# Optimization experiments

Measured on AMD Instinct MI355X. Metric: run time of the kernel, lower is better.

## Reference

```python
import jax, jax.numpy as jnp
import numpy as np

D_K = 64
EPS = 1e-6


def setup_inputs() -> dict:
    key = jax.random.key(0)
    ks = jax.random.split(key, 6)
    B, S, D2, DV = 4, 2048, 1024, 64
    q = jax.random.normal(ks[0], (B, S, D2), dtype=jnp.float32)
    k = jax.random.normal(ks[1], (B, S, D2), dtype=jnp.float32)
    v = jax.random.normal(ks[2], (B, S, D2), dtype=jnp.float32)
    mask = jax.random.randint(ks[3], (B, S, S), 0, 2) == 1
    V = jax.random.normal(ks[4], (1, DV), dtype=jnp.float32)
    fc_w = jax.random.normal(ks[5], (D2, DV), dtype=jnp.float32) * (1.0 / np.sqrt(DV))
    fc_b = jnp.zeros((D2,), dtype=jnp.float32)
    ln_g = jnp.ones((D2,), dtype=jnp.float32)
    ln_b = jnp.zeros((D2,), dtype=jnp.float32)
    return {"q": q, "k": k, "v": v, "mask": mask, "V": V,
            "fc_w": fc_w, "fc_b": fc_b, "ln_g": ln_g, "ln_b": ln_b}


def _layer_norm(x, g, b):
    mu = jnp.mean(x, axis=-1, keepdims=True)
    var = jnp.var(x, axis=-1, keepdims=True)
    return (x - mu) * jax.lax.rsqrt(var + EPS) * g + b


def reference(q, k, v, mask, V, fc_w, fc_b, ln_g, ln_b):
    residual = q
    qn = _layer_norm(q, ln_g, ln_b)
    # scaled dot-product scores (no softmax in this variant)
    attn = jnp.einsum('bsd,btd->bst', qn / jnp.sqrt(jnp.float32(D_K)), k)
    attn = jnp.where(mask, 0.0, attn)  # masked_fill with 0
    # v_ = V broadcast over (batch, seq, key); attn @ v_ == row-sum outer V
    output = jnp.sum(attn, axis=-1, keepdims=True) * V  # [B,S,d_v]
    output = output @ fc_w.T + fc_b                     # [B,S,2*d_model]
    output = output + residual
    return (output, attn)
```

## Files before the change

kernel.cpp:

```cpp
#include <hip/hip_runtime.h>
#include <hip/hip_bf16.h>
#include <cstdint>

#define S_LEN 2048
#define D2_   1024
#define DV_   64
#define NB_   4

typedef __bf16 bf16x8 __attribute__((ext_vector_type(8)));
typedef float  f32x16 __attribute__((ext_vector_type(16)));

__device__ __forceinline__ unsigned short f2bf(float f) {
  union { float f; unsigned int u; } v; v.f = f;
  unsigned int r = v.u + 0x7fffu + ((v.u >> 16) & 1u);
  return (unsigned short)(r >> 16);
}

__device__ __forceinline__ void async16(const unsigned short* g, unsigned short* l) {
  __builtin_amdgcn_global_load_lds(
      (__attribute__((address_space(1))) void*)g,
      (__attribute__((address_space(3))) void*)l,
      16, 0, 0);
}

__global__ void __launch_bounds__(256) prep_kernel(
    const float* __restrict__ q, const float* __restrict__ k,
    const float* __restrict__ gam, const float* __restrict__ bet,
    const float* __restrict__ V, const float* __restrict__ fw,
    unsigned short* __restrict__ qn, unsigned short* __restrict__ kb,
    float* __restrict__ w2, float* __restrict__ rowsum) {
  const int row = blockIdx.x;
  const int t = threadIdx.x;

  if (row < 32) rowsum[row * 256 + t] = 0.0f;

  const float4 x = ((const float4*)(q + (size_t)row * D2_))[t];
  float s  = x.x + x.y + x.z + x.w;
  float ss = x.x * x.x + x.y * x.y + x.z * x.z + x.w * x.w;
  #pragma unroll
  for (int o = 32; o > 0; o >>= 1) { s += __shfl_down(s, o); ss += __shfl_down(ss, o); }
  __shared__ float red[8];
  if ((t & 63) == 0) { red[t >> 6] = s; red[(t >> 6) + 4] = ss; }
  __syncthreads();
  const float tot  = red[0] + red[1] + red[2] + red[3];
  const float tots = red[4] + red[5] + red[6] + red[7];
  const float mu  = tot * (1.0f / D2_);
  const float var = tots * (1.0f / D2_) - mu * mu;
  const float rs  = rsqrtf(var + 1e-6f) * 0.125f;
  const float4 gv = ((const float4*)gam)[t];
  const float4 bv = ((const float4*)bet)[t];
  ushort4 o4;
  o4.x = f2bf((x.x - mu) * rs * gv.x + 0.125f * bv.x);
  o4.y = f2bf((x.y - mu) * rs * gv.y + 0.125f * bv.y);
  o4.z = f2bf((x.z - mu) * rs * gv.z + 0.125f * bv.z);
  o4.w = f2bf((x.w - mu) * rs * gv.w + 0.125f * bv.w);
  ((ushort4*)(qn + (size_t)row * D2_))[t] = o4;

  const float4 kx = ((const float4*)(k + (size_t)row * D2_))[t];
  ushort4 k4;
  k4.x = f2bf(kx.x); k4.y = f2bf(kx.y); k4.z = f2bf(kx.z); k4.w = f2bf(kx.w);
  ((ushort4*)(kb + (size_t)row * D2_))[t] = k4;

  if (row < 4) {
    const int d = row * 256 + t;
    const float4* r  = (const float4*)(fw + (size_t)d * DV_);
    const float4* vv = (const float4*)V;
    float acc = 0.f;
    #pragma unroll
    for (int j = 0; j < 16; ++j) {
      const float4 a = r[j], b = vv[j];
      acc += a.x * b.x + a.y * b.y + a.z * b.z + a.w * b.w;
    }
    w2[d] = acc;
  }
}

__global__ void __launch_bounds__(256) attn_gemm_kernel(
    const unsigned short* __restrict__ qn,
    const unsigned short* __restrict__ kb,
    const int* __restrict__ mask,
    float* __restrict__ attn,
    float* __restrict__ rowsum) {
  __shared__ __align__(16) unsigned short Asm_[128 * 32];
  __shared__ __align__(16) unsigned short Bsm_[128 * 32];

  const int t  = threadIdx.x;
  const int bn = blockIdx.x * 128;
  const int bm = blockIdx.y * 128;
  const int bt = blockIdx.z;

  const int srow_ = t >> 2;
  const int kg_   = (t & 3) ^ (srow_ & 3);
  const unsigned short* gA = qn + ((size_t)bt * S_LEN + bm + srow_) * D2_ + kg_ * 8;
  const unsigned short* gB = kb + ((size_t)bt * S_LEN + bn + srow_) * D2_ + kg_ * 8;
  unsigned short* lA = Asm_ + t * 8;
  unsigned short* lB = Bsm_ + t * 8;

  const int lane = t & 63;
  const int w    = t >> 6;
  const int wm   = (w >> 1) * 64;
  const int wn   = (w & 1) * 64;
  const int col  = lane & 31;
  const int half = lane >> 5;

  const int x0 = (half ^ (lane & 3)) * 8;
  const int x1 = ((2 + half) ^ (lane & 3)) * 8;

  f32x16 acc[2][2] = {};

  for (int k0 = 0; k0 < D2_; k0 += 32) {
    async16(gA, lA);
    async16(gA + 64 * D2_, lA + 2048);
    async16(gB, lB);
    async16(gB + 64 * D2_, lB + 2048);
    gA += 32; gB += 32;
    __syncthreads();

    bf16x8 af[2][2], bfv[2][2];
    #pragma unroll
    for (int f = 0; f < 2; ++f) {
      const int ra = (wm + f * 32 + col) * 32;
      const int rb = (wn + f * 32 + col) * 32;
      af[f][0]  = *(const bf16x8*)(Asm_ + ra + x0);
      af[f][1]  = *(const bf16x8*)(Asm_ + ra + x1);
      bfv[f][0] = *(const bf16x8*)(Bsm_ + rb + x0);
      bfv[f][1] = *(const bf16x8*)(Bsm_ + rb + x1);
    }
    #pragma unroll
    for (int s = 0; s < 2; ++s)
      #pragma unroll
      for (int fm = 0; fm < 2; ++fm)
        #pragma unroll
        for (int fn = 0; fn < 2; ++fn)
          acc[fm][fn] = __builtin_amdgcn_mfma_f32_32x32x16_bf16(
              af[fm][s], bfv[fn][s], acc[fm][fn], 0, 0, 0);
    __syncthreads();
  }

  #pragma unroll
  for (int fm = 0; fm < 2; ++fm) {
    #pragma unroll
    for (int r = 0; r < 16; ++r) {
      const int srow = bm + wm + fm * 32 + (r & 3) + 8 * (r >> 2) + 4 * half;
      const size_t base = ((size_t)bt * S_LEN + srow) * S_LEN + bn + wn;
      float v0 = acc[fm][0][r];
      float v1 = acc[fm][1][r];
      v0 = mask[base + col] ? 0.0f : v0;
      v1 = mask[base + 32 + col] ? 0.0f : v1;
      attn[base + col]      = v0;
      attn[base + 32 + col] = v1;
      float s = v0 + v1;
      #pragma unroll
      for (int o = 16; o > 0; o >>= 1) s += __shfl_down(s, o, 32);
      if (col == 0) atomicAdd(rowsum + (size_t)bt * S_LEN + srow, s);
    }
  }
}

__global__ void __launch_bounds__(256) out_kernel(
    const float* __restrict__ rowsum, const float* __restrict__ q,
    const float* __restrict__ w2, const float* __restrict__ fcb,
    float* __restrict__ out) {
  const int row = blockIdx.x;
  const int t = threadIdx.x;
  const float rs = rowsum[row];
  const float4 wv = ((const float4*)w2)[t];
  const float4 bv = ((const float4*)fcb)[t];
  const float4 qv = ((const float4*)(q + (size_t)row * D2_))[t];
  float4 o4;
  o4.x = rs * wv.x + bv.x + qv.x;
  o4.y = rs * wv.y + bv.y + qv.y;
  o4.z = rs * wv.z + bv.z + qv.z;
  o4.w = rs * wv.w + bv.w + qv.w;
  ((float4*)(out + (size_t)row * D2_))[t] = o4;
}

extern "C" void kernel_launch(void* const* d_in, const int* in_sizes, int n_in,
                              void* d_out, int out_size, void* d_ws, size_t ws_size,
                              hipStream_t stream) {
  (void)in_sizes; (void)n_in; (void)out_size; (void)ws_size;
  const float* q    = (const float*)d_in[0];
  const float* k    = (const float*)d_in[1];
  const int*   mask = (const int*)d_in[3];
  const float* V    = (const float*)d_in[4];
  const float* fw   = (const float*)d_in[5];
  const float* fcb  = (const float*)d_in[6];
  const float* lg   = (const float*)d_in[7];
  const float* lb   = (const float*)d_in[8];

  float* out  = (float*)d_out;
  float* attn = out + (size_t)NB_ * S_LEN * D2_;

  unsigned short* qn = (unsigned short*)out;
  unsigned short* kb = qn + (size_t)NB_ * S_LEN * D2_;
  float* w2     = (float*)d_ws;
  float* rowsum = w2 + D2_;

  prep_kernel<<<NB_ * S_LEN, 256, 0, stream>>>(q, k, lg, lb, V, fw, qn, kb, w2, rowsum);
  attn_gemm_kernel<<<dim3(S_LEN / 128, S_LEN / 128, NB_), 256, 0, stream>>>(qn, kb, mask, attn, rowsum);
  out_kernel<<<NB_ * S_LEN, 256, 0, stream>>>(rowsum, q, w2, fcb, out);
}
```

Baseline: 320.5 us.

## Switch attention GEMM to 16x16x32 MFMA with K=64 tiles and vectorized epilogue

Replaces the 32x32x16 MFMA tiling with 16x16x32 bf16 MFMAs and operands swapped so each lane holds four consecutive columns of a row. The K tile grows from 32 to 64 with an 8-way XOR swizzle, and launch bounds request 4 blocks per CU. The epilogue now reads the mask and writes attn as int4/float4 vectors and cuts the atomics per row. The aim is fewer barriers per K step and wider, coalesced stores for the output-bound epilogue. The cost is a larger LDS footprint and more accumulator registers per lane.

```diff
diff --git a/kernel.cpp b/kernel.cpp
--- a/kernel.cpp
+++ b/kernel.cpp
@@ -8,7 +8,7 @@
 #define NB_   4
 
 typedef __bf16 bf16x8 __attribute__((ext_vector_type(8)));
-typedef float  f32x16 __attribute__((ext_vector_type(16)));
+typedef float  f32x4  __attribute__((ext_vector_type(4)));
 
 __device__ __forceinline__ unsigned short f2bf(float f) {
   union { float f; unsigned int u; } v; v.f = f;
@@ -75,85 +75,84 @@
   }
 }
 
-__global__ void __launch_bounds__(256) attn_gemm_kernel(
+__global__ void __launch_bounds__(256, 4) attn_gemm_kernel(
     const unsigned short* __restrict__ qn,
     const unsigned short* __restrict__ kb,
     const int* __restrict__ mask,
     float* __restrict__ attn,
     float* __restrict__ rowsum) {
-  __shared__ __align__(16) unsigned short Asm_[128 * 32];
-  __shared__ __align__(16) unsigned short Bsm_[128 * 32];
+  __shared__ __align__(16) unsigned short Asm_[128 * 64];
+  __shared__ __align__(16) unsigned short Bsm_[128 * 64];
 
   const int t  = threadIdx.x;
   const int bn = blockIdx.x * 128;
   const int bm = blockIdx.y * 128;
   const int bt = blockIdx.z;
 
-  const int srow_ = t >> 2;
-  const int kg_   = (t & 3) ^ (srow_ & 3);
+  const int srow_ = t >> 3;
+  const int kg_   = (t & 7) ^ (srow_ & 7);
   const unsigned short* gA = qn + ((size_t)bt * S_LEN + bm + srow_) * D2_ + kg_ * 8;
   const unsigned short* gB = kb + ((size_t)bt * S_LEN + bn + srow_) * D2_ + kg_ * 8;
   unsigned short* lA = Asm_ + t * 8;
   unsigned short* lB = Bsm_ + t * 8;
 
   const int lane = t & 63;
-  const int w    = t >> 6;
-  const int wm   = (w >> 1) * 64;
-  const int wn   = (w & 1) * 64;
-  const int col  = lane & 31;
-  const int half = lane >> 5;
-
-  const int x0 = (half ^ (lane & 3)) * 8;
-  const int x1 = ((2 + half) ^ (lane & 3)) * 8;
-
-  f32x16 acc[2][2] = {};
-
-  for (int k0 = 0; k0 < D2_; k0 += 32) {
-    async16(gA, lA);
-    async16(gA + 64 * D2_, lA + 2048);
-    async16(gB, lB);
-    async16(gB + 64 * D2_, lB + 2048);
-    gA += 32; gB += 32;
+  const int w  = t >> 6;
+  const int wm = (w >> 1) * 64;
+  const int wn = (w & 1) * 64;
+  const int lr = lane & 15;
+  const int lg = lane >> 4;
+
+  f32x4 acc[4][4] = {};
+
+  for (int k0 = 0; k0 < D2_; k0 += 64) {
+    #pragma unroll
+    for (int j = 0; j < 4; ++j) {
+      async16(gA + j * 32 * D2_, lA + j * 2048);
+      async16(gB + j * 32 * D2_, lB + j * 2048);
+    }
+    gA += 64; gB += 64;
     __syncthreads();
 
-    bf16x8 af[2][2], bfv[2][2];
-    #pragma unroll
-    for (int f = 0; f < 2; ++f) {
-      const int ra = (wm + f * 32 + col) * 32;
-      const int rb = (wn + f * 32 + col) * 32;
-      af[f][0]  = *(const bf16x8*)(Asm_ + ra + x0);
-      af[f][1]  = *(const bf16x8*)(Asm_ + ra + x1);
-      bfv[f][0] = *(const bf16x8*)(Bsm_ + rb + x0);
-      bfv[f][1] = *(const bf16x8*)(Bsm_ + rb + x1);
-    }
-    #pragma unroll
-    for (int s = 0; s < 2; ++s)
+    #pragma unroll
+    for (int ks = 0; ks < 2; ++ks) {
+      bf16x8 af[4], bfv[4];
       #pragma unroll
-      for (int fm = 0; fm < 2; ++fm)
+      for (int f = 0; f < 4; ++f) {
+        const int sl = ((ks << 2) + lg) ^ (lr & 7);
+        af[f]  = *(const bf16x8*)(Asm_ + (wm + f * 16 + lr) * 64 + sl * 8);
+        bfv[f] = *(const bf16x8*)(Bsm_ + (wn + f * 16 + lr) * 64 + sl * 8);
+      }
+      #pragma unroll
+      for (int fm = 0; fm < 4; ++fm)
         #pragma unroll
-        for (int fn = 0; fn < 2; ++fn)
-          acc[fm][fn] = __builtin_amdgcn_mfma_f32_32x32x16_bf16(
-              af[fm][s], bfv[fn][s], acc[fm][fn], 0, 0, 0);
+        for (int fn = 0; fn < 4; ++fn)
+          acc[fm][fn] = __builtin_amdgcn_mfma_f32_16x16x32_bf16(
+              bfv[fn], af[fm], acc[fm][fn], 0, 0, 0);
+    }
     __syncthreads();
   }
 
   #pragma unroll
-  for (int fm = 0; fm < 2; ++fm) {
-    #pragma unroll
-    for (int r = 0; r < 16; ++r) {
-      const int srow = bm + wm + fm * 32 + (r & 3) + 8 * (r >> 2) + 4 * half;
-      const size_t base = ((size_t)bt * S_LEN + srow) * S_LEN + bn + wn;
-      float v0 = acc[fm][0][r];
-      float v1 = acc[fm][1][r];
-      v0 = mask[base + col] ? 0.0f : v0;
-      v1 = mask[base + 32 + col] ? 0.0f : v1;
-      attn[base + col]      = v0;
-      attn[base + 32 + col] = v1;
-      float s = v0 + v1;
-      #pragma unroll
-      for (int o = 16; o > 0; o >>= 1) s += __shfl_down(s, o, 32);
-      if (col == 0) atomicAdd(rowsum + (size_t)bt * S_LEN + srow, s);
-    }
+  for (int fm = 0; fm < 4; ++fm) {
+    const int m = bm + wm + fm * 16 + lr;
+    const size_t rowbase = ((size_t)bt * S_LEN + m) * S_LEN;
+    float s = 0.f;
+    #pragma unroll
+    for (int fn = 0; fn < 4; ++fn) {
+      const int n0 = bn + wn + fn * 16 + lg * 4;
+      const int4 mk = *(const int4*)(mask + rowbase + n0);
+      float4 v;
+      v.x = mk.x ? 0.0f : acc[fm][fn][0];
+      v.y = mk.y ? 0.0f : acc[fm][fn][1];
+      v.z = mk.z ? 0.0f : acc[fm][fn][2];
+      v.w = mk.w ? 0.0f : acc[fm][fn][3];
+      *(float4*)(attn + rowbase + n0) = v;
+      s += v.x + v.y + v.z + v.w;
+    }
+    s += __shfl_xor(s, 16);
+    s += __shfl_xor(s, 32);
+    if (lane < 16) atomicAdd(rowsum + (size_t)bt * S_LEN + m, s);
   }
 }
 
```

Result: faster. 275.3 us (-14.1%).
